# Performance work log

Measured on AMD Instinct MI355X. Metric: run time of the kernel, lower is better.

The kernel has to match this reference:

```python
import jax, jax.numpy as jnp
import numpy as np

B, T, CIN = 8, 4096, 512
GROUP, ENTRY = 2, 320
COUT = 512
D = COUT // GROUP  # per-group codebook dim = 256


def setup_inputs() -> dict:
    key = jax.random.key(0)
    k_x, k_w, k_cb, k_g = jax.random.split(key, 4)
    x = jax.random.normal(k_x, (B, T, CIN), dtype=jnp.float32)
    # weight_proj: Linear(in_channel, group*entry)
    Wp = jax.random.normal(k_w, (GROUP * ENTRY, CIN), dtype=jnp.float32) * (1.0 / np.sqrt(CIN))
    bp = jnp.zeros((GROUP * ENTRY,), dtype=jnp.float32)
    # stacked codebooks: [group, entry, out_channel//group]
    codebooks = jax.random.normal(k_cb, (GROUP, ENTRY, D), dtype=jnp.float32)
    # pre-sampled gumbel noise (torch gumbel_softmax samples this internally)
    gumbel = jax.random.gumbel(k_g, (B, T, GROUP * ENTRY), dtype=jnp.float32)
    return {"x": x, "Wp": Wp, "bp": bp, "codebooks": codebooks, "gumbel": gumbel}


def reference(x, Wp, bp, codebooks, gumbel):
    # weight_proj
    logits = jnp.einsum('btc,ec->bte', x, Wp) + bp          # [B,T,group*entry]
    # gumbel_softmax(tau=1, hard=False, dim=-1): softmax over full group*entry axis
    y = jax.nn.softmax(logits + gumbel, axis=-1)            # [B,T,group*entry]
    # chunk into groups -> contiguous reshape matches torch.chunk
    yg = y.reshape(B, T, GROUP, ENTRY)                      # [B,T,G,E]
    # per-group matmul against codebook weights, then concat over groups
    out = jnp.einsum('btge,ged->btgd', yg, codebooks)       # [B,T,G,D]
    return out.reshape(B, T, GROUP * D)                     # [B,T,out_channel]
```

## Files before the change

### kernel.cpp

```cpp
#include <hip/hip_runtime.h>
#include <stdint.h>

#define BT     32768
#define CIN    512
#define NE     640
#define ENTRY  320
#define DD     256
#define MROWS  32
#define TPB    256

using bf16x8 = __attribute__((ext_vector_type(8))) short;
using f32x4  = __attribute__((ext_vector_type(4))) float;

#define S_OFF      40960
#define SMEM_BYTES 41088

__device__ __forceinline__ unsigned short f2b(float f) {
    union { float f; uint32_t u; } v; v.f = f;
    uint32_t u = v.u;
    return (unsigned short)((u + 0x7FFFu + ((u >> 16) & 1u)) >> 16);
}

__global__ void prep_kernel(const float* __restrict__ Wp, const float* __restrict__ cb,
                            unsigned short* __restrict__ WpB2, unsigned short* __restrict__ cbT2) {
    int i = blockIdx.x * blockDim.x + threadIdx.x;
    if (i < NE * CIN) {
        int ks  = i / 20480;
        int rem = i - ks * 20480;
        int e   = rem >> 5;
        int kk  = rem & 31;
        WpB2[i] = f2b(Wp[e * CIN + ks * 32 + kk]);
    } else {
        int o = i - NE * CIN;
        if (o < 2 * ENTRY * DD) {
            int kk = o & 31;
            int t  = o >> 5;
            int n  = t & 255;
            int t2 = t >> 8;
            int ks = t2 % 10;
            int g  = t2 / 10;
            cbT2[o] = f2b(cb[(g * ENTRY + ks * 32 + kk) * DD + n]);
        }
    }
}

__global__ __launch_bounds__(TPB, 3) void fused_kernel(
    const float* __restrict__ x, const float* __restrict__ bp,
    const float* __restrict__ gum, const unsigned short* __restrict__ WpB2,
    const unsigned short* __restrict__ cbT2, float* __restrict__ out) {

    extern __shared__ char smem[];
    float* sS = (float*)(smem + S_OFF);

    const int tid = threadIdx.x;
    const int w  = tid >> 6;
    const int l  = tid & 63;
    const int q  = l >> 4;
    const int ln = l & 15;
    const int rowbase = blockIdx.x * MROWS;
    const int swz = (ln & 7) << 4;

    if (tid < MROWS) sS[tid] = 0.0f;

    {
        const int ar  = tid >> 3;
        const int akq = tid & 7;
        const float* xrow = x + (size_t)(rowbase + ar) * CIN + akq * 4;
        const int abase = ar * 1024;
        const int aswz  = (ar & 7) << 4;
#pragma unroll
        for (int c = 0; c < 16; ++c) {
            float4 xv = *(const float4*)(xrow + c * 32);
            ushort4 hv;
            hv.x = f2b(xv.x); hv.y = f2b(xv.y); hv.z = f2b(xv.z); hv.w = f2b(xv.w);
            *(ushort4*)(smem + abase + ((c * 64 + akq * 8) ^ aswz)) = hv;
        }
    }
    __syncthreads();

    f32x4 acc1[2][10];
    const f32x4 fz = {0.f, 0.f, 0.f, 0.f};
#pragma unroll
    for (int rt = 0; rt < 2; ++rt)
#pragma unroll
        for (int ct = 0; ct < 10; ++ct) acc1[rt][ct] = fz;

    const int blane = ln * 32 + q * 8;

#pragma unroll 1
    for (int ks = 0; ks < 16; ++ks) {
        const unsigned short* pk = WpB2 + ks * (NE * 32) + (w * 160) * 32 + blane;
        const int at = (ks * 64 + q * 16) ^ swz;
        bf16x8 af0 = *(const bf16x8*)(smem + ln * 1024 + at);
        bf16x8 af1 = *(const bf16x8*)(smem + ln * 1024 + 16384 + at);
#pragma unroll
        for (int ct = 0; ct < 10; ++ct) {
            bf16x8 bfr = *(const bf16x8*)(pk + ct * 512);
            acc1[0][ct] = __builtin_amdgcn_mfma_f32_16x16x32_bf16(af0, bfr, acc1[0][ct], 0, 0, 0);
            acc1[1][ct] = __builtin_amdgcn_mfma_f32_16x16x32_bf16(af1, bfr, acc1[1][ct], 0, 0, 0);
        }
    }
    __syncthreads();

    float bpv[10];
#pragma unroll
    for (int ct = 0; ct < 10; ++ct) bpv[ct] = bp[w * 160 + ct * 16 + ln];

#pragma unroll
    for (int ri = 0; ri < 8; ++ri) {
        int rt = ri >> 2, r = ri & 3;
        int row = rt * 16 + q * 4 + r;
        const float* pg = gum + (size_t)(rowbase + row) * NE + w * 160 + ln;
        int ybase = row * 1280;
        int yswz  = (row & 7) << 4;
        float p = 0.f;
#pragma unroll
        for (int ct = 0; ct < 10; ++ct) {
            int col = w * 160 + ct * 16 + ln;
            float v = acc1[rt][ct][r] + bpv[ct] + pg[ct * 16];
            float e = __expf(v);
            *(unsigned short*)(smem + ybase + ((col * 2) ^ yswz)) = f2b(e);
            p += e;
        }
        p += __shfl_xor(p, 1);
        p += __shfl_xor(p, 2);
        p += __shfl_xor(p, 4);
        p += __shfl_xor(p, 8);
        if (ln == 0) atomicAdd(&sS[row], p);
    }
    __syncthreads();

    f32x4 acc2[2][8];
#pragma unroll
    for (int rt = 0; rt < 2; ++rt)
#pragma unroll
        for (int ct = 0; ct < 8; ++ct) acc2[rt][ct] = fz;

    const int g  = w >> 1;
    const int nb = (w & 1) * 128;

#pragma unroll 1
    for (int ks = 0; ks < 10; ++ks) {
        const unsigned short* pk = cbT2 + ((size_t)(g * 10 + ks) * 256 + nb) * 32 + blane;
        const int at = (g * 640 + ks * 64 + q * 16) ^ swz;
        bf16x8 af0 = *(const bf16x8*)(smem + ln * 1280 + at);
        bf16x8 af1 = *(const bf16x8*)(smem + ln * 1280 + 20480 + at);
#pragma unroll
        for (int ct = 0; ct < 8; ++ct) {
            bf16x8 bfr = *(const bf16x8*)(pk + ct * 512);
            acc2[0][ct] = __builtin_amdgcn_mfma_f32_16x16x32_bf16(af0, bfr, acc2[0][ct], 0, 0, 0);
            acc2[1][ct] = __builtin_amdgcn_mfma_f32_16x16x32_bf16(af1, bfr, acc2[1][ct], 0, 0, 0);
        }
    }

#pragma unroll
    for (int rt = 0; rt < 2; ++rt) {
#pragma unroll
        for (int r = 0; r < 4; ++r) {
            int row = rt * 16 + q * 4 + r;
            float inv = 1.0f / sS[row];
            size_t orow = (size_t)(rowbase + row) * 512;
#pragma unroll
            for (int ct = 0; ct < 8; ++ct) {
                int col = g * 256 + nb + ct * 16 + ln;
                out[orow + col] = acc2[rt][ct][r] * inv;
            }
        }
    }
}

extern "C" void kernel_launch(void* const* d_in, const int* in_sizes, int n_in,
                              void* d_out, int out_size, void* d_ws, size_t ws_size,
                              hipStream_t stream) {
    const float* x   = (const float*)d_in[0];
    const float* Wp  = (const float*)d_in[1];
    const float* bp  = (const float*)d_in[2];
    const float* cb  = (const float*)d_in[3];
    const float* gum = (const float*)d_in[4];
    float* out = (float*)d_out;

    unsigned short* WpB2 = (unsigned short*)d_ws;
    unsigned short* cbT2 = WpB2 + NE * CIN;

    int prep_total = NE * CIN + 2 * ENTRY * DD;
    prep_kernel<<<(prep_total + 255) / 256, 256, 0, stream>>>(Wp, cb, WpB2, cbT2);

    fused_kernel<<<dim3(BT / MROWS), dim3(TPB), SMEM_BYTES, stream>>>(x, bp, gum, WpB2, cbT2, out);
}
```

Measured before the change: 274.0 us.

## Double-buffer MFMA operand loads and double rows per block with eight waves

Raises the block tile from 32 to 64 rows and the block size from 256 to 512 threads, so each block runs eight waves in a 2x4 grid and every weight/codebook fragment fetched from global memory serves twice as many rows. Both GEMM loops are unrolled by two with ping-pong register buffers, so the next k-step's B fragments and LDS A fragments are loaded while the current MFMAs run. The codebook fragments for the second GEMM are prefetched before the softmax phase. The cost is higher register pressure from the extra buffers, double the LDS per block (about 82 KB), and fewer resident blocks (launch bounds 2 instead of 3).

```diff
diff --git a/kernel.cpp b/kernel.cpp
--- a/kernel.cpp
+++ b/kernel.cpp
@@ -6,14 +6,14 @@
 #define NE     640
 #define ENTRY  320
 #define DD     256
-#define MROWS  32
-#define TPB    256
+#define MROWS  64
+#define TPB    512
 
 using bf16x8 = __attribute__((ext_vector_type(8))) short;
 using f32x4  = __attribute__((ext_vector_type(4))) float;
 
-#define S_OFF      40960
-#define SMEM_BYTES 41088
+#define S_OFF      81920
+#define SMEM_BYTES 82176
 
 __device__ __forceinline__ unsigned short f2b(float f) {
     union { float f; uint32_t u; } v; v.f = f;
@@ -44,7 +44,9 @@
     }
 }
 
-__global__ __launch_bounds__(TPB, 3) void fused_kernel(
+#define MFMA16(d, a, b) d = __builtin_amdgcn_mfma_f32_16x16x32_bf16(a, b, d, 0, 0, 0)
+
+__global__ __launch_bounds__(TPB, 2) void fused_kernel(
     const float* __restrict__ x, const float* __restrict__ bp,
     const float* __restrict__ gum, const unsigned short* __restrict__ WpB2,
     const unsigned short* __restrict__ cbT2, float* __restrict__ out) {
@@ -57,6 +59,8 @@
     const int l  = tid & 63;
     const int q  = l >> 4;
     const int ln = l & 15;
+    const int wr = w >> 2;
+    const int wc = w & 3;
     const int rowbase = blockIdx.x * MROWS;
     const int swz = (ln & 7) << 4;
 
@@ -86,37 +90,72 @@
         for (int ct = 0; ct < 10; ++ct) acc1[rt][ct] = fz;
 
     const int blane = ln * 32 + q * 8;
+    const unsigned short* bptr = WpB2 + (wc * 160) * 32 + blane;
+    const int aB = (wr * 32 + ln) * 1024;
+
+    bf16x8 pA[10], pB[10];
+    bf16x8 aA0, aA1, aB0, aB1;
+#pragma unroll
+    for (int ct = 0; ct < 10; ++ct) pA[ct] = *(const bf16x8*)(bptr + ct * 512);
+    {
+        const int at = (q * 16) ^ swz;
+        aA0 = *(const bf16x8*)(smem + aB + at);
+        aA1 = *(const bf16x8*)(smem + aB + 16384 + at);
+    }
 
 #pragma unroll 1
-    for (int ks = 0; ks < 16; ++ks) {
-        const unsigned short* pk = WpB2 + ks * (NE * 32) + (w * 160) * 32 + blane;
-        const int at = (ks * 64 + q * 16) ^ swz;
-        bf16x8 af0 = *(const bf16x8*)(smem + ln * 1024 + at);
-        bf16x8 af1 = *(const bf16x8*)(smem + ln * 1024 + 16384 + at);
+    for (int ks2 = 0; ks2 < 16; ks2 += 2) {
+        {
+            const unsigned short* pk = bptr + (ks2 + 1) * 20480;
+#pragma unroll
+            for (int ct = 0; ct < 10; ++ct) pB[ct] = *(const bf16x8*)(pk + ct * 512);
+            const int at = ((ks2 + 1) * 64 + q * 16) ^ swz;
+            aB0 = *(const bf16x8*)(smem + aB + at);
+            aB1 = *(const bf16x8*)(smem + aB + 16384 + at);
+        }
 #pragma unroll
         for (int ct = 0; ct < 10; ++ct) {
-            bf16x8 bfr = *(const bf16x8*)(pk + ct * 512);
-            acc1[0][ct] = __builtin_amdgcn_mfma_f32_16x16x32_bf16(af0, bfr, acc1[0][ct], 0, 0, 0);
-            acc1[1][ct] = __builtin_amdgcn_mfma_f32_16x16x32_bf16(af1, bfr, acc1[1][ct], 0, 0, 0);
+            MFMA16(acc1[0][ct], aA0, pA[ct]);
+            MFMA16(acc1[1][ct], aA1, pA[ct]);
+        }
+        if (ks2 + 2 < 16) {
+            const unsigned short* pk = bptr + (ks2 + 2) * 20480;
+#pragma unroll
+            for (int ct = 0; ct < 10; ++ct) pA[ct] = *(const bf16x8*)(pk + ct * 512);
+            const int at = ((ks2 + 2) * 64 + q * 16) ^ swz;
+            aA0 = *(const bf16x8*)(smem + aB + at);
+            aA1 = *(const bf16x8*)(smem + aB + 16384 + at);
+        }
+#pragma unroll
+        for (int ct = 0; ct < 10; ++ct) {
+            MFMA16(acc1[0][ct], aB0, pB[ct]);
+            MFMA16(acc1[1][ct], aB1, pB[ct]);
         }
     }
     __syncthreads();
 
+    const int g  = wc >> 1;
+    const int nb = (wc & 1) * 128;
+    const unsigned short* cptr = cbT2 + (size_t)g * 81920 + nb * 32 + blane;
+    bf16x8 cA[8], cB[8];
+#pragma unroll
+    for (int ct = 0; ct < 8; ++ct) cA[ct] = *(const bf16x8*)(cptr + ct * 512);
+
     float bpv[10];
 #pragma unroll
-    for (int ct = 0; ct < 10; ++ct) bpv[ct] = bp[w * 160 + ct * 16 + ln];
+    for (int ct = 0; ct < 10; ++ct) bpv[ct] = bp[wc * 160 + ct * 16 + ln];
 
 #pragma unroll
     for (int ri = 0; ri < 8; ++ri) {
         int rt = ri >> 2, r = ri & 3;
-        int row = rt * 16 + q * 4 + r;
-        const float* pg = gum + (size_t)(rowbase + row) * NE + w * 160 + ln;
-        int ybase = row * 1280;
-        int yswz  = (row & 7) << 4;
+        int lrow = wr * 32 + rt * 16 + q * 4 + r;
+        const float* pg = gum + (size_t)(rowbase + lrow) * NE + wc * 160 + ln;
+        int ybase = lrow * 1280;
+        int yswz  = (lrow & 7) << 4;
         float p = 0.f;
 #pragma unroll
         for (int ct = 0; ct < 10; ++ct) {
-            int col = w * 160 + ct * 16 + ln;
+            int col = wc * 160 + ct * 16 + ln;
             float v = acc1[rt][ct][r] + bpv[ct] + pg[ct * 16];
             float e = __expf(v);
             *(unsigned short*)(smem + ybase + ((col * 2) ^ yswz)) = f2b(e);
@@ -126,7 +165,7 @@
         p += __shfl_xor(p, 2);
         p += __shfl_xor(p, 4);
         p += __shfl_xor(p, 8);
-        if (ln == 0) atomicAdd(&sS[row], p);
+        if (ln == 0) atomicAdd(&sS[lrow], p);
     }
     __syncthreads();
 
@@ -136,20 +175,41 @@
 #pragma unroll
         for (int ct = 0; ct < 8; ++ct) acc2[rt][ct] = fz;
 
-    const int g  = w >> 1;
-    const int nb = (w & 1) * 128;
+    const int yB = (wr * 32 + ln) * 1280;
+    bf16x8 yA0, yA1, yB0, yB1;
+    {
+        const int at = (g * 640 + q * 16) ^ swz;
+        yA0 = *(const bf16x8*)(smem + yB + at);
+        yA1 = *(const bf16x8*)(smem + yB + 20480 + at);
+    }
 
 #pragma unroll 1
-    for (int ks = 0; ks < 10; ++ks) {
-        const unsigned short* pk = cbT2 + ((size_t)(g * 10 + ks) * 256 + nb) * 32 + blane;
-        const int at = (g * 640 + ks * 64 + q * 16) ^ swz;
-        bf16x8 af0 = *(const bf16x8*)(smem + ln * 1280 + at);
-        bf16x8 af1 = *(const bf16x8*)(smem + ln * 1280 + 20480 + at);
+    for (int ks2 = 0; ks2 < 10; ks2 += 2) {
+        {
+            const unsigned short* pk = cptr + (ks2 + 1) * 8192;
+#pragma unroll
+            for (int ct = 0; ct < 8; ++ct) cB[ct] = *(const bf16x8*)(pk + ct * 512);
+            const int at = (g * 640 + (ks2 + 1) * 64 + q * 16) ^ swz;
+            yB0 = *(const bf16x8*)(smem + yB + at);
+            yB1 = *(const bf16x8*)(smem + yB + 20480 + at);
+        }
 #pragma unroll
         for (int ct = 0; ct < 8; ++ct) {
-            bf16x8 bfr = *(const bf16x8*)(pk + ct * 512);
-            acc2[0][ct] = __builtin_amdgcn_mfma_f32_16x16x32_bf16(af0, bfr, acc2[0][ct], 0, 0, 0);
-            acc2[1][ct] = __builtin_amdgcn_mfma_f32_16x16x32_bf16(af1, bfr, acc2[1][ct], 0, 0, 0);
+            MFMA16(acc2[0][ct], yA0, cA[ct]);
+            MFMA16(acc2[1][ct], yA1, cA[ct]);
+        }
+        if (ks2 + 2 < 10) {
+            const unsigned short* pk = cptr + (ks2 + 2) * 8192;
+#pragma unroll
+            for (int ct = 0; ct < 8; ++ct) cA[ct] = *(const bf16x8*)(pk + ct * 512);
+            const int at = (g * 640 + (ks2 + 2) * 64 + q * 16) ^ swz;
+            yA0 = *(const bf16x8*)(smem + yB + at);
+            yA1 = *(const bf16x8*)(smem + yB + 20480 + at);
+        }
+#pragma unroll
+        for (int ct = 0; ct < 8; ++ct) {
+            MFMA16(acc2[0][ct], yB0, cB[ct]);
+            MFMA16(acc2[1][ct], yB1, cB[ct]);
         }
     }
 
@@ -157,9 +217,9 @@
     for (int rt = 0; rt < 2; ++rt) {
 #pragma unroll
         for (int r = 0; r < 4; ++r) {
-            int row = rt * 16 + q * 4 + r;
-            float inv = 1.0f / sS[row];
-            size_t orow = (size_t)(rowbase + row) * 512;
+            int lrow = wr * 32 + rt * 16 + q * 4 + r;
+            float inv = 1.0f / sS[lrow];
+            size_t orow = (size_t)(rowbase + lrow) * 512;
 #pragma unroll
             for (int ct = 0; ct < 8; ++ct) {
                 int col = g * 256 + nb + ct * 16 + ln;
```

Measured after the change: 250.7 us. -8.5%, faster.
